# Performance work log

Hardware: AMD Instinct MI355X
Metric: run time of the kernel (lower is better)

The kernel has to match this reference:

```python
import jax, jax.numpy as jnp
import numpy as np


def setup_inputs() -> dict:
    key = jax.random.key(0)
    ks = jax.random.split(key, 5)
    B, n_sites, d_bond, d_phys = 8192, 2048, 8, 2
    sr = n_sites // 2  # single_rank
    x = jax.random.normal(ks[0], (B, n_sites, d_phys), dtype=jnp.float32)
    scale = 0.01
    left_b = scale * jax.random.normal(ks[1], (d_bond, d_phys), dtype=jnp.float32)
    left = scale * jax.random.normal(ks[2], (sr - 1, d_bond, d_bond, d_phys), dtype=jnp.float32)
    right = scale * jax.random.normal(ks[3], (sr - 1, d_bond, d_bond, d_phys), dtype=jnp.float32)
    right_b = scale * jax.random.normal(ks[4], (d_bond, d_phys), dtype=jnp.float32)
    return {"x": x, "left_b": left_b, "left": left, "right": right, "right_b": right_b}


def reference(x, left_b, left, right, right_b):
    # x: [B, n_sites, d_phys]; left/right: [sr-1, bond, bond, d_phys]; boundaries: [bond, d_phys]
    n_sites = x.shape[1]
    sr = n_sites // 2

    # In-place slice normalizations performed at the top of call()
    left_b = left_b.at[2].set(left_b[2] / jnp.linalg.norm(left_b[2]))
    left = left.at[3].set(left[3] / jnp.linalg.norm(left[3]))
    right = right.at[3].set(right[3] / jnp.linalg.norm(right[3]))
    right_b = right_b.at[2].set(right_b[2] / jnp.linalg.norm(right_b[2]))

    # Left half: boundary phys contraction -> [B, bond]
    lvec = jnp.einsum("ap,kp->ka", left_b, x[:, 0])
    # Middle left: contract site-stack and phys axes -> [B, bond, bond]
    Lmat = jnp.einsum("sabp,ksp->kab", left, x[:, 1:sr])
    l = jnp.einsum("ka,kab->kb", lvec, Lmat)  # contract lb_n[0]^ln[1]

    # Right half (mirror)
    rvec = jnp.einsum("ap,kp->ka", right_b, x[:, n_sites - 1])
    Rmat = jnp.einsum("sabp,ksp->kab", right, x[:, sr : n_sites - 1])
    r = jnp.einsum("ka,kab->kb", rvec, Rmat)

    # Join halves: ln[2]^rn[2] -> scalar per sample, shape [B]
    return jnp.einsum("kb,kb->k", l, r)
```

## Files before the change

### kernel.cpp

```cpp
#include <hip/hip_runtime.h>
#include <hip/hip_bf16.h>

typedef __bf16  bf16x8  __attribute__((ext_vector_type(8)));
typedef float   floatx4 __attribute__((ext_vector_type(4)));

#define ROWLEN      4096
#define B_SAMPLES   8192
#define FRAG_ELEMS  (2*64*4*64*8)


__global__ __launch_bounds__(256) void repack_kernel(
    const float* __restrict__ left, const float* __restrict__ right,
    __bf16* __restrict__ wfrag)
{
    __shared__ float norms[2];
    const int tid  = threadIdx.x;
    const int wv   = tid >> 6;
    const int ln   = tid & 63;

    if (wv < 2) {
        const float* W = (wv == 0) ? left : right;
        float a = W[384 + ln], b = W[384 + 64 + ln];
        float s = a * a + b * b;
        s += __shfl_xor(s, 1);  s += __shfl_xor(s, 2);  s += __shfl_xor(s, 4);
        s += __shfl_xor(s, 8);  s += __shfl_xor(s, 16); s += __shfl_xor(s, 32);
        if (ln == 0) norms[wv] = 1.0f / sqrtf(s);
    }
    __syncthreads();
    const float invL = norms[0];
    const float invR = norms[1];

    const int g    = (int)(blockIdx.x * 256) + tid;
    const int lane = g & 63;
    const int nt   = (g >> 6) & 3;
    const int t    = (g >> 8) & 63;
    const int h    = (g >> 14) & 1;
    const int kk0  = t * 32 + (lane >> 4) * 8;
    const int n    = nt * 16 + (lane & 15);
    const int a    = n >> 3, bb = n & 7;
    const float* W = (h == 0) ? left : right;

    bf16x8 frag;
#pragma unroll
    for (int si = 0; si < 4; ++si) {
        const int kk = kk0 + si * 2;
        int s;  bool valid;
        if (h == 0) { s = (kk >> 1) - 1; valid = (kk >= 2); }
        else        { s = (kk >> 1);     valid = (s < 1023); }
        float w0 = 0.f, w1 = 0.f;
        if (valid) {
            const float* wp = W + ((s * 8 + a) * 8 + bb) * 2;
            w0 = wp[0]; w1 = wp[1];
            if (s == 3) { const float sc = (h == 0) ? invL : invR; w0 *= sc; w1 *= sc; }
        }
        frag[si * 2]     = (__bf16)w0;
        frag[si * 2 + 1] = (__bf16)w1;
    }
    ((bf16x8*)wfrag)[g] = frag;
}

__global__ __launch_bounds__(512, 2) void mps_main_kernel(
    const float* __restrict__ x, const __bf16* __restrict__ wfrag,
    const float* __restrict__ left_b, const float* __restrict__ right_b,
    float* __restrict__ out)
{
    __shared__ float lds[2][4][32][65];
    const int tid  = threadIdx.x;
    const int wid  = tid >> 6;
    const int lane = tid & 63;
    const int h    = wid & 1;
    const int c    = wid >> 1;
    const int mcol = lane & 15;
    const int q    = lane >> 4;
    const int blk  = blockIdx.x;

    const float* arow0 = x + (size_t)(blk * 32 + mcol) * ROWLEN
                           + h * 2048 + c * 512 + q * 8;
    const float* arow1 = arow0 + (size_t)16 * ROWLEN;
    const bf16x8* bbase = (const bf16x8*)wfrag
                          + ((size_t)(h * 64 + c * 16) * 4) * 64 + lane;

    floatx4 accA0 = {0.f,0.f,0.f,0.f}, accA1 = {0.f,0.f,0.f,0.f};
    floatx4 accA2 = {0.f,0.f,0.f,0.f}, accA3 = {0.f,0.f,0.f,0.f};
    floatx4 accB0 = {0.f,0.f,0.f,0.f}, accB1 = {0.f,0.f,0.f,0.f};
    floatx4 accB2 = {0.f,0.f,0.f,0.f}, accB3 = {0.f,0.f,0.f,0.f};

#pragma unroll 4
    for (int tl = 0; tl < 16; ++tl) {
        const floatx4* ap0 = (const floatx4*)(arow0 + tl * 32);
        const floatx4* ap1 = (const floatx4*)(arow1 + tl * 32);
        const floatx4 a0 = __builtin_nontemporal_load(ap0);
        const floatx4 a1 = __builtin_nontemporal_load(ap0 + 1);
        const floatx4 b0 = __builtin_nontemporal_load(ap1);
        const floatx4 b1 = __builtin_nontemporal_load(ap1 + 1);
        bf16x8 af0, af1;
        af0[0] = (__bf16)a0[0]; af0[1] = (__bf16)a0[1];
        af0[2] = (__bf16)a0[2]; af0[3] = (__bf16)a0[3];
        af0[4] = (__bf16)a1[0]; af0[5] = (__bf16)a1[1];
        af0[6] = (__bf16)a1[2]; af0[7] = (__bf16)a1[3];
        af1[0] = (__bf16)b0[0]; af1[1] = (__bf16)b0[1];
        af1[2] = (__bf16)b0[2]; af1[3] = (__bf16)b0[3];
        af1[4] = (__bf16)b1[0]; af1[5] = (__bf16)b1[1];
        af1[6] = (__bf16)b1[2]; af1[7] = (__bf16)b1[3];
        const bf16x8* bp = bbase + (size_t)tl * 256;
        const bf16x8 w0 = bp[0], w1 = bp[64], w2 = bp[128], w3 = bp[192];
        accA0 = __builtin_amdgcn_mfma_f32_16x16x32_bf16(af0, w0, accA0, 0, 0, 0);
        accB0 = __builtin_amdgcn_mfma_f32_16x16x32_bf16(af1, w0, accB0, 0, 0, 0);
        accA1 = __builtin_amdgcn_mfma_f32_16x16x32_bf16(af0, w1, accA1, 0, 0, 0);
        accB1 = __builtin_amdgcn_mfma_f32_16x16x32_bf16(af1, w1, accB1, 0, 0, 0);
        accA2 = __builtin_amdgcn_mfma_f32_16x16x32_bf16(af0, w2, accA2, 0, 0, 0);
        accB2 = __builtin_amdgcn_mfma_f32_16x16x32_bf16(af1, w2, accB2, 0, 0, 0);
        accA3 = __builtin_amdgcn_mfma_f32_16x16x32_bf16(af0, w3, accA3, 0, 0, 0);
        accB3 = __builtin_amdgcn_mfma_f32_16x16x32_bf16(af1, w3, accB3, 0, 0, 0);
    }

#pragma unroll
    for (int i = 0; i < 4; ++i) {
        const int r0 = q * 4 + i;
        lds[h][c][r0][ 0 + mcol] = accA0[i];
        lds[h][c][r0][16 + mcol] = accA1[i];
        lds[h][c][r0][32 + mcol] = accA2[i];
        lds[h][c][r0][48 + mcol] = accA3[i];
        lds[h][c][16 + r0][ 0 + mcol] = accB0[i];
        lds[h][c][16 + r0][16 + mcol] = accB1[i];
        lds[h][c][16 + r0][32 + mcol] = accB2[i];
        lds[h][c][16 + r0][48 + mcol] = accB3[i];
    }
    __syncthreads();

    if (tid < 256) {
        const int mm = tid >> 3;
        const int b  = tid & 7;
        const size_t k = (size_t)blk * 32 + mm;
        const float* xr = x + k * ROWLEN;
        const float x0 = xr[0],    x1 = xr[1];
        const float y0 = xr[4094], y1 = xr[4095];
        const float lbn = 1.0f / sqrtf(left_b[4]*left_b[4] + left_b[5]*left_b[5]);
        const float rbn = 1.0f / sqrtf(right_b[4]*right_b[4] + right_b[5]*right_b[5]);
        float l = 0.f, r = 0.f;
#pragma unroll
        for (int a = 0; a < 8; ++a) {
            float lv = left_b[a*2]  * x0 + left_b[a*2+1]  * x1;
            float rv = right_b[a*2] * y0 + right_b[a*2+1] * y1;
            if (a == 2) { lv *= lbn; rv *= rbn; }
            const int n = a * 8 + b;
            const float ls = lds[0][0][mm][n] + lds[0][1][mm][n]
                           + lds[0][2][mm][n] + lds[0][3][mm][n];
            const float rs = lds[1][0][mm][n] + lds[1][1][mm][n]
                           + lds[1][2][mm][n] + lds[1][3][mm][n];
            l += lv * ls;
            r += rv * rs;
        }
        float vv = l * r;
        vv += __shfl_xor(vv, 1);
        vv += __shfl_xor(vv, 2);
        vv += __shfl_xor(vv, 4);
        if (b == 0) out[k] = vv;
    }
}

extern "C" void kernel_launch(void* const* d_in, const int* in_sizes, int n_in,
                              void* d_out, int out_size, void* d_ws, size_t ws_size,
                              hipStream_t stream)
{
    const float* x       = (const float*)d_in[0];
    const float* left_b  = (const float*)d_in[1];
    const float* left    = (const float*)d_in[2];
    const float* right   = (const float*)d_in[3];
    const float* right_b = (const float*)d_in[4];

    __bf16* wfrag = (__bf16*)d_ws;
    float*  out   = (float*)d_out;

    hipLaunchKernelGGL(repack_kernel, dim3(128), dim3(256), 0, stream,
                       left, right, wfrag);
    hipLaunchKernelGGL(mps_main_kernel, dim3(B_SAMPLES / 32), dim3(512), 0, stream,
                       x, wfrag, left_b, right_b, out);
}
```

Baseline: 198.5 us.

## Stage x tiles into LDS via async global_load_lds with double buffering

Each 32-row block of x is now copied into a double-buffered LDS staging area in 512-column chunks using direct global-to-LDS loads, with an XOR swizzle to avoid bank conflicts. Wavefronts then read their MFMA operands from LDS, and the next chunk's load is issued while the current one is computed. The goal is fully coalesced row loads overlapped with compute, in place of strided per-lane global loads. In exchange it needs 128KB of LDS, which lowers occupancy, adds a barrier per chunk, and leaves half the waves idle in each chunk.

```diff
diff --git a/kernel.cpp b/kernel.cpp
--- a/kernel.cpp
+++ b/kernel.cpp
@@ -6,7 +6,13 @@
 
 #define ROWLEN      4096
 #define B_SAMPLES   8192
-#define FRAG_ELEMS  (2*64*4*64*8)
+
+typedef const __attribute__((address_space(1))) void* gas1_t;
+typedef __attribute__((address_space(3))) void*       las3_t;
+
+__device__ __forceinline__ void stage16(const float* g, float* l) {
+    __builtin_amdgcn_global_load_lds((gas1_t)g, (las3_t)l, 16, 0, 0);
+}
 
 
 __global__ __launch_bounds__(256) void repack_kernel(
@@ -64,67 +70,100 @@
     const float* __restrict__ left_b, const float* __restrict__ right_b,
     float* __restrict__ out)
 {
-    __shared__ float lds[2][4][32][65];
+    __shared__ float smem[32768];
     const int tid  = threadIdx.x;
     const int wid  = tid >> 6;
     const int lane = tid & 63;
-    const int h    = wid & 1;
-    const int c    = wid >> 1;
+    const int hw   = wid & 1;
+    const int v    = wid >> 1;
     const int mcol = lane & 15;
     const int q    = lane >> 4;
+    const int p    = lane & 7;
     const int blk  = blockIdx.x;
 
-    const float* arow0 = x + (size_t)(blk * 32 + mcol) * ROWLEN
-                           + h * 2048 + c * 512 + q * 8;
-    const float* arow1 = arow0 + (size_t)16 * ROWLEN;
-    const bf16x8* bbase = (const bf16x8*)wfrag
-                          + ((size_t)(h * 64 + c * 16) * 4) * 64 + lane;
+    const float* xblk = x + (size_t)blk * 32 * ROWLEN;
+
+#pragma unroll
+    for (int i = 0; i < 4; ++i) {
+        const int r = 4 * wid + i;
+        const float* gp = xblk + (size_t)r * ROWLEN + ((lane ^ (r & 7)) * 4);
+        stage16(gp,       &smem[r * 512]);
+        stage16(gp + 256, &smem[r * 512 + 256]);
+    }
+    __syncthreads();
 
     floatx4 accA0 = {0.f,0.f,0.f,0.f}, accA1 = {0.f,0.f,0.f,0.f};
     floatx4 accA2 = {0.f,0.f,0.f,0.f}, accA3 = {0.f,0.f,0.f,0.f};
     floatx4 accB0 = {0.f,0.f,0.f,0.f}, accB1 = {0.f,0.f,0.f,0.f};
     floatx4 accB2 = {0.f,0.f,0.f,0.f}, accB3 = {0.f,0.f,0.f,0.f};
 
-#pragma unroll 4
-    for (int tl = 0; tl < 16; ++tl) {
-        const floatx4* ap0 = (const floatx4*)(arow0 + tl * 32);
-        const floatx4* ap1 = (const floatx4*)(arow1 + tl * 32);
-        const floatx4 a0 = __builtin_nontemporal_load(ap0);
-        const floatx4 a1 = __builtin_nontemporal_load(ap0 + 1);
-        const floatx4 b0 = __builtin_nontemporal_load(ap1);
-        const floatx4 b1 = __builtin_nontemporal_load(ap1 + 1);
-        bf16x8 af0, af1;
-        af0[0] = (__bf16)a0[0]; af0[1] = (__bf16)a0[1];
-        af0[2] = (__bf16)a0[2]; af0[3] = (__bf16)a0[3];
-        af0[4] = (__bf16)a1[0]; af0[5] = (__bf16)a1[1];
-        af0[6] = (__bf16)a1[2]; af0[7] = (__bf16)a1[3];
-        af1[0] = (__bf16)b0[0]; af1[1] = (__bf16)b0[1];
-        af1[2] = (__bf16)b0[2]; af1[3] = (__bf16)b0[3];
-        af1[4] = (__bf16)b1[0]; af1[5] = (__bf16)b1[1];
-        af1[6] = (__bf16)b1[2]; af1[7] = (__bf16)b1[3];
-        const bf16x8* bp = bbase + (size_t)tl * 256;
-        const bf16x8 w0 = bp[0], w1 = bp[64], w2 = bp[128], w3 = bp[192];
-        accA0 = __builtin_amdgcn_mfma_f32_16x16x32_bf16(af0, w0, accA0, 0, 0, 0);
-        accB0 = __builtin_amdgcn_mfma_f32_16x16x32_bf16(af1, w0, accB0, 0, 0, 0);
-        accA1 = __builtin_amdgcn_mfma_f32_16x16x32_bf16(af0, w1, accA1, 0, 0, 0);
-        accB1 = __builtin_amdgcn_mfma_f32_16x16x32_bf16(af1, w1, accB1, 0, 0, 0);
-        accA2 = __builtin_amdgcn_mfma_f32_16x16x32_bf16(af0, w2, accA2, 0, 0, 0);
-        accB2 = __builtin_amdgcn_mfma_f32_16x16x32_bf16(af1, w2, accB2, 0, 0, 0);
-        accA3 = __builtin_amdgcn_mfma_f32_16x16x32_bf16(af0, w3, accA3, 0, 0, 0);
-        accB3 = __builtin_amdgcn_mfma_f32_16x16x32_bf16(af1, w3, accB3, 0, 0, 0);
-    }
-
-#pragma unroll
-    for (int i = 0; i < 4; ++i) {
-        const int r0 = q * 4 + i;
-        lds[h][c][r0][ 0 + mcol] = accA0[i];
-        lds[h][c][r0][16 + mcol] = accA1[i];
-        lds[h][c][r0][32 + mcol] = accA2[i];
-        lds[h][c][r0][48 + mcol] = accA3[i];
-        lds[h][c][16 + r0][ 0 + mcol] = accB0[i];
-        lds[h][c][16 + r0][16 + mcol] = accB1[i];
-        lds[h][c][16 + r0][32 + mcol] = accB2[i];
-        lds[h][c][16 + r0][48 + mcol] = accB3[i];
+#pragma unroll
+    for (int ch = 0; ch < 8; ++ch) {
+        const int cbuf = (ch & 1) * 16384;
+        if (ch < 7) {
+            const int cn     = ch + 1;
+            const int coloff = (cn & 1) * 2048 + (cn >> 1) * 512;
+            const int nbuf   = (cn & 1) * 16384;
+#pragma unroll
+            for (int i = 0; i < 4; ++i) {
+                const int r = 4 * wid + i;
+                const float* gp = xblk + (size_t)r * ROWLEN + coloff
+                                + ((lane ^ (r & 7)) * 4);
+                stage16(gp,       &smem[nbuf + r * 512]);
+                stage16(gp + 256, &smem[nbuf + r * 512 + 256]);
+            }
+        }
+        if ((ch & 1) == hw) {
+            const int cc = ch >> 1;
+            const float* sA = &smem[cbuf + mcol * 512];
+            const float* sB = &smem[cbuf + (16 + mcol) * 512];
+            const bf16x8* bp0 = (const bf16x8*)wfrag
+                + ((size_t)((hw * 64 + cc * 16 + 4 * v) * 4)) * 64 + lane;
+#pragma unroll
+            for (int ti = 0; ti < 4; ++ti) {
+                const int g0 = (4 * v + ti) * 8 + 2 * q;
+                const floatx4 a0 = *(const floatx4*)&sA[((g0    ) ^ p) * 4];
+                const floatx4 a1 = *(const floatx4*)&sA[((g0 + 1) ^ p) * 4];
+                const floatx4 b0 = *(const floatx4*)&sB[((g0    ) ^ p) * 4];
+                const floatx4 b1 = *(const floatx4*)&sB[((g0 + 1) ^ p) * 4];
+                bf16x8 af0, af1;
+                af0[0] = (__bf16)a0[0]; af0[1] = (__bf16)a0[1];
+                af0[2] = (__bf16)a0[2]; af0[3] = (__bf16)a0[3];
+                af0[4] = (__bf16)a1[0]; af0[5] = (__bf16)a1[1];
+                af0[6] = (__bf16)a1[2]; af0[7] = (__bf16)a1[3];
+                af1[0] = (__bf16)b0[0]; af1[1] = (__bf16)b0[1];
+                af1[2] = (__bf16)b0[2]; af1[3] = (__bf16)b0[3];
+                af1[4] = (__bf16)b1[0]; af1[5] = (__bf16)b1[1];
+                af1[6] = (__bf16)b1[2]; af1[7] = (__bf16)b1[3];
+                const bf16x8* bp = bp0 + (size_t)ti * 256;
+                const bf16x8 w0 = bp[0], w1 = bp[64], w2 = bp[128], w3 = bp[192];
+                accA0 = __builtin_amdgcn_mfma_f32_16x16x32_bf16(af0, w0, accA0, 0, 0, 0);
+                accB0 = __builtin_amdgcn_mfma_f32_16x16x32_bf16(af1, w0, accB0, 0, 0, 0);
+                accA1 = __builtin_amdgcn_mfma_f32_16x16x32_bf16(af0, w1, accA1, 0, 0, 0);
+                accB1 = __builtin_amdgcn_mfma_f32_16x16x32_bf16(af1, w1, accB1, 0, 0, 0);
+                accA2 = __builtin_amdgcn_mfma_f32_16x16x32_bf16(af0, w2, accA2, 0, 0, 0);
+                accB2 = __builtin_amdgcn_mfma_f32_16x16x32_bf16(af1, w2, accB2, 0, 0, 0);
+                accA3 = __builtin_amdgcn_mfma_f32_16x16x32_bf16(af0, w3, accA3, 0, 0, 0);
+                accB3 = __builtin_amdgcn_mfma_f32_16x16x32_bf16(af1, w3, accB3, 0, 0, 0);
+            }
+        }
+        __syncthreads();
+    }
+
+    {
+        const int base = (hw * 4 + v) * 32;
+#pragma unroll
+        for (int i = 0; i < 4; ++i) {
+            const int r0 = q * 4 + i;
+            smem[(base + r0) * 65 +  0 + mcol] = accA0[i];
+            smem[(base + r0) * 65 + 16 + mcol] = accA1[i];
+            smem[(base + r0) * 65 + 32 + mcol] = accA2[i];
+            smem[(base + r0) * 65 + 48 + mcol] = accA3[i];
+            smem[(base + 16 + r0) * 65 +  0 + mcol] = accB0[i];
+            smem[(base + 16 + r0) * 65 + 16 + mcol] = accB1[i];
+            smem[(base + 16 + r0) * 65 + 32 + mcol] = accB2[i];
+            smem[(base + 16 + r0) * 65 + 48 + mcol] = accB3[i];
+        }
     }
     __syncthreads();
 
@@ -144,10 +183,10 @@
             float rv = right_b[a*2] * y0 + right_b[a*2+1] * y1;
             if (a == 2) { lv *= lbn; rv *= rbn; }
             const int n = a * 8 + b;
-            const float ls = lds[0][0][mm][n] + lds[0][1][mm][n]
-                           + lds[0][2][mm][n] + lds[0][3][mm][n];
-            const float rs = lds[1][0][mm][n] + lds[1][1][mm][n]
-                           + lds[1][2][mm][n] + lds[1][3][mm][n];
+            const float ls = smem[((0*4+0)*32 + mm)*65 + n] + smem[((0*4+1)*32 + mm)*65 + n]
+                           + smem[((0*4+2)*32 + mm)*65 + n] + smem[((0*4+3)*32 + mm)*65 + n];
+            const float rs = smem[((1*4+0)*32 + mm)*65 + n] + smem[((1*4+1)*32 + mm)*65 + n]
+                           + smem[((1*4+2)*32 + mm)*65 + n] + smem[((1*4+3)*32 + mm)*65 + n];
             l += lv * ls;
             r += rv * rs;
         }
```

After: 214.4 us. 1.08x slower.
